# Performance work log

Measured on AMD Instinct MI355X. Metric: run time of the kernel, lower is better.

## Reference

```python
import jax, jax.numpy as jnp
import numpy as np

DN = ('NCDHW', 'OIDHW', 'NCDHW')

def conv3d(x, w, b):
    # kernel (1,3,3), stride 1, padding (0,1,1)
    y = jax.lax.conv_general_dilated(x, w, window_strides=(1, 1, 1),
                                     padding=[(0, 0), (1, 1), (1, 1)],
                                     dimension_numbers=DN)
    return y + b[None, :, None, None, None]

def setup_inputs() -> dict:
    key = jax.random.key(0)
    ks = jax.random.split(key, 9)
    B, C, S, H, W = 16, 64, 64, 32, 32
    Cd = C // 2
    fan = C * 9
    sc = 1.0 / np.sqrt(fan)
    x = jax.random.normal(ks[0], (B, C, S, H, W), jnp.float32)
    wq = jax.random.normal(ks[1], (Cd, C, 1, 3, 3), jnp.float32) * sc
    bq = jax.random.normal(ks[2], (Cd,), jnp.float32) * sc
    wk = jax.random.normal(ks[3], (Cd, C, 1, 3, 3), jnp.float32) * sc
    bk = jax.random.normal(ks[4], (Cd,), jnp.float32) * sc
    wv = jax.random.normal(ks[5], (Cd, C, 1, 3, 3), jnp.float32) * sc
    bv = jax.random.normal(ks[6], (Cd,), jnp.float32) * sc
    wo = jax.random.normal(ks[7], (C, Cd, 1, 3, 3), jnp.float32) * (1.0 / np.sqrt(Cd * 9))
    bo = jax.random.normal(ks[8], (C,), jnp.float32) * (1.0 / np.sqrt(Cd * 9))
    return {"x": x, "wq": wq, "bq": bq, "wk": wk, "bk": bk,
            "wv": wv, "bv": bv, "wo": wo, "bo": bo}

def reference(x, wq, bq, wk, bk, wv, bv, wo, bo):
    B, C, S, H, W = x.shape
    scale = (H * W) ** (-0.5)
    q = conv3d(x, wq, bq).reshape(B, -1, S, H * W)  # (B, Cd, S, HW)
    k = conv3d(x, wk, bk).reshape(B, -1, S, H * W)
    v = conv3d(x, wv, bv).reshape(B, -1, S, H * W)
    # per-channel attention over sequence dim with sigmoid gate
    attn = jax.nn.sigmoid(jnp.einsum('bcsf,bctf->bcst', q, k) * scale)  # (B, Cd, S, S)
    out = jnp.einsum('bcst,bctf->bcsf', attn, v)  # (B, Cd, S, HW)
    out = out.reshape(B, -1, S, H, W)
    return conv3d(out, wo, bo)
```

## Files before the change

kernel.cpp:

```cpp
#include <hip/hip_runtime.h>
#include <hip/hip_bf16.h>

#define BB   16
#define CC   64
#define SS   64
#define HWHW 1024
#define CD   32
#define QELEMS (BB * CD * SS * HWHW)

typedef unsigned short ushort_t;
typedef __attribute__((ext_vector_type(8)))  short bf16x8;
typedef __attribute__((ext_vector_type(16))) float f32x16;

static __device__ inline float bf2f(ushort_t u) {
    union { float f; unsigned int i; } v;
    v.i = ((unsigned int)u) << 16;
    return v.f;
}
static __device__ inline ushort_t f2bf(float f) {
    union { float f; unsigned int i; } v;
    v.f = f;
    unsigned int x = v.i;
    return (ushort_t)((x + 0x7fffu + ((x >> 16) & 1u)) >> 16);
}

__global__ __launch_bounds__(256) void pack_weights(
    const float* __restrict__ wq, const float* __restrict__ wk,
    const float* __restrict__ wv, const float* __restrict__ wo,
    ushort_t* __restrict__ wt, ushort_t* __restrict__ wt2)
{
    const int d = blockIdx.x * 256 + threadIdx.x;
    if (d < 9 * 96 * 64) {
        const int tap = d / (96 * 64);
        const int rem = d % (96 * 64);
        const int oc  = rem >> 6;
        const int c   = rem & 63;
        const float* wsrc = (oc < 32) ? wq : (oc < 64) ? wk : wv;
        const int ocl = oc & 31;
        wt[d] = f2bf(wsrc[((size_t)ocl * 64 + c) * 9 + tap]);
    }
    const int d2 = d - 9 * 96 * 64;
    if (d2 >= 0 && d2 < 9 * 64 * 32) {
        const int tap = d2 / (64 * 32);
        const int rem = d2 % (64 * 32);
        const int oc  = rem >> 5;
        const int c   = rem & 31;
        wt2[d2] = f2bf(wo[((size_t)oc * 32 + c) * 9 + tap]);
    }
}

__global__ __launch_bounds__(256) void transpose_x(
    const float* __restrict__ x, ushort_t* __restrict__ xT)
{
    __shared__ ushort_t t[64][132];

    const int bs  = blockIdx.x;
    const int b   = bs >> 6;
    const int s   = bs & 63;
    const int tid = threadIdx.x;
    const float* xb = x + ((size_t)b * CC * SS + s) * HWHW;
    ushort_t*    xo = xT + (size_t)bs * HWHW * CC;

    for (int fc = 0; fc < 8; ++fc) {
        __syncthreads();
#pragma unroll
        for (int i = 0; i < 8; ++i) {
            const int u  = tid + i * 256;
            const int c  = u >> 5;
            const int f4 = u & 31;
            const float4 v = *(const float4*)(xb + (size_t)c * SS * HWHW + fc * 128 + f4 * 4);
            const unsigned int lo = (unsigned int)f2bf(v.x) | ((unsigned int)f2bf(v.y) << 16);
            const unsigned int hi = (unsigned int)f2bf(v.z) | ((unsigned int)f2bf(v.w) << 16);
            *(uint2*)&t[c][f4 * 4] = make_uint2(lo, hi);
        }
        __syncthreads();
#pragma unroll
        for (int i = 0; i < 4; ++i) {
            const int u  = tid + i * 256;
            const int px = u >> 3;
            const int cg = (u & 7) * 8;
            bf16x8 vv;
#pragma unroll
            for (int j = 0; j < 8; ++j) vv[j] = (short)t[cg + j][px];
            *(bf16x8*)(xo + (size_t)(fc * 128 + px) * CC + cg) = vv;
        }
    }
}

__global__ __launch_bounds__(256) void transpose_att(
    const ushort_t* __restrict__ att, ushort_t* __restrict__ attT)
{
    __shared__ ushort_t t[32][260];

    const int bs  = blockIdx.x;
    const int b   = bs >> 6;
    const int s   = bs & 63;
    const int tid = threadIdx.x;
    const ushort_t* ab = att + ((size_t)b * CD * SS + s) * HWHW;
    ushort_t*       ao = attT + (size_t)bs * HWHW * CD;

    for (int fc = 0; fc < 4; ++fc) {
        __syncthreads();
#pragma unroll
        for (int i = 0; i < 8; ++i) {
            const int u  = tid + i * 256;
            const int c  = u >> 6;
            const int f4 = u & 63;
            const ushort4 v = *(const ushort4*)(ab + (size_t)c * SS * HWHW + fc * 256 + f4 * 4);
            *(ushort4*)&t[c][f4 * 4] = v;
        }
        __syncthreads();
#pragma unroll
        for (int i = 0; i < 4; ++i) {
            const int u  = tid + i * 256;
            const int px = u >> 2;
            const int cg = (u & 3) * 8;
            bf16x8 vv;
#pragma unroll
            for (int j = 0; j < 8; ++j) vv[j] = (short)t[cg + j][px];
            *(bf16x8*)(ao + (size_t)(fc * 256 + px) * CD + cg) = vv;
        }
    }
}

__global__ __launch_bounds__(256) void conv_qkv_mfma(
    const ushort_t* __restrict__ xT,
    const ushort_t* __restrict__ wt,
    const float* __restrict__ bq, const float* __restrict__ bk,
    const float* __restrict__ bv,
    ushort_t* __restrict__ qkv)
{
    __shared__ ushort_t xs[10][34][72];

    const int tid   = threadIdx.x;
    const int bs    = blockIdx.x >> 2;
    const int chunk = blockIdx.x & 3;
    const int b     = bs >> 6;
    const int s     = bs & 63;
    const int h0    = chunk * 8;

    if (tid < 160) {
        const int r    = tid >> 4;
        const int rest = tid & 15;
        const int col  = (rest >> 3) ? 33 : 0;
        const int c0   = (rest & 7) << 3;
        bf16x8 z = {0, 0, 0, 0, 0, 0, 0, 0};
        *(bf16x8*)&xs[r][col][c0] = z;
    }

    const ushort_t* xb = xT + (size_t)bs * HWHW * CC;
    {
        const int w  = tid >> 3;
        const int cg = (tid & 7) * 8;
#pragma unroll
        for (int it = 0; it < 10; ++it) {
            const int h = h0 - 1 + it;
            bf16x8 v = {0, 0, 0, 0, 0, 0, 0, 0};
            if (h >= 0 && h < 32)
                v = *(const bf16x8*)(xb + (size_t)(h * 32 + w) * CC + cg);
            *(bf16x8*)&xs[it][1 + w][cg] = v;
        }
    }
    __syncthreads();

    const int wvid = tid >> 6;
    const int lane = tid & 63;
    const int ln   = lane & 31;
    const int lh   = lane >> 5;
    const int nt0  = wvid * 2;

    f32x16 acc[3][2];
#pragma unroll
    for (int m = 0; m < 3; ++m)
#pragma unroll
        for (int n = 0; n < 2; ++n)
#pragma unroll
            for (int i = 0; i < 16; ++i) acc[m][n][i] = 0.f;

#pragma unroll 1
    for (int tap = 0; tap < 9; ++tap) {
        const int dh = tap / 3;
        const int dw = tap % 3;
        const ushort_t* wtap = wt + (size_t)tap * 96 * 64;
#pragma unroll
        for (int kc = 0; kc < 4; ++kc) {
            const int c0 = kc * 16 + lh * 8;
            const bf16x8 a0 = *(const bf16x8*)(wtap + (((size_t)ln      ) << 6) + c0);
            const bf16x8 a1 = *(const bf16x8*)(wtap + (((size_t)ln + 32 ) << 6) + c0);
            const bf16x8 a2 = *(const bf16x8*)(wtap + (((size_t)ln + 64 ) << 6) + c0);
            const bf16x8 b0 = *(const bf16x8*)&xs[nt0 + dh    ][ln + dw][c0];
            const bf16x8 b1 = *(const bf16x8*)&xs[nt0 + 1 + dh][ln + dw][c0];
            acc[0][0] = __builtin_amdgcn_mfma_f32_32x32x16_bf16(a0, b0, acc[0][0], 0, 0, 0);
            acc[0][1] = __builtin_amdgcn_mfma_f32_32x32x16_bf16(a0, b1, acc[0][1], 0, 0, 0);
            acc[1][0] = __builtin_amdgcn_mfma_f32_32x32x16_bf16(a1, b0, acc[1][0], 0, 0, 0);
            acc[1][1] = __builtin_amdgcn_mfma_f32_32x32x16_bf16(a1, b1, acc[1][1], 0, 0, 0);
            acc[2][0] = __builtin_amdgcn_mfma_f32_32x32x16_bf16(a2, b0, acc[2][0], 0, 0, 0);
            acc[2][1] = __builtin_amdgcn_mfma_f32_32x32x16_bf16(a2, b1, acc[2][1], 0, 0, 0);
        }
    }

    const float* biases[3] = {bq, bk, bv};
#pragma unroll
    for (int mt = 0; mt < 3; ++mt) {
        const float* bptr = biases[mt];
        ushort_t* dst = qkv + (size_t)mt * QELEMS + (((size_t)b * CD) * SS + s) * HWHW;
#pragma unroll
        for (int ntl = 0; ntl < 2; ++ntl) {
            const int gp = (h0 + nt0 + ntl) * 32 + ln;
#pragma unroll
            for (int r = 0; r < 16; ++r) {
                const int m = (r & 3) + 8 * (r >> 2) + 4 * lh;
                const float val = acc[mt][ntl][r] + bptr[m];
                dst[(size_t)m * SS * HWHW + gp] = f2bf(val);
            }
        }
    }
}

__global__ __launch_bounds__(256) void attn_kernel(ushort_t* __restrict__ qkv)
{
    __shared__ float    scb[64][65];
    __shared__ ushort_t qch[64][132];
    __shared__ ushort_t kch[64][132];

    const int tid = threadIdx.x;
    const int bc  = blockIdx.x;
    ushort_t* qbase = qkv + (size_t)bc * SS * HWHW;
    const ushort_t* kbase = qbase + QELEMS;
    const ushort_t* vbase = qbase + 2 * (size_t)QELEMS;

    const int ty = tid >> 4, tx = tid & 15;
    const int sy = ty * 4, sx = tx * 4;

    float acc[4][4];
#pragma unroll
    for (int i = 0; i < 4; ++i)
#pragma unroll
        for (int j = 0; j < 4; ++j) acc[i][j] = 0.0f;

    for (int fc = 0; fc < 8; ++fc) {
        __syncthreads();
#pragma unroll
        for (int u = 0; u < 8; ++u) {
            const int unit = tid + u * 256;
            const int row  = unit >> 5;
            const int col  = (unit & 31) * 4;
            const ushort4 qa = *(const ushort4*)(qbase + (size_t)row * HWHW + fc * 128 + col);
            const ushort4 ka = *(const ushort4*)(kbase + (size_t)row * HWHW + fc * 128 + col);
            *(ushort4*)&qch[row][col] = qa;
            *(ushort4*)&kch[row][col] = ka;
        }
        __syncthreads();

        for (int f = 0; f < 128; f += 2) {
            float q0[4], q1[4], k0[4], k1[4];
#pragma unroll
            for (int i = 0; i < 4; ++i) {
                const unsigned int qp = *(const unsigned int*)&qch[sy + i][f];
                q0[i] = bf2f((ushort_t)(qp & 0xffffu));
                q1[i] = bf2f((ushort_t)(qp >> 16));
                const unsigned int kp = *(const unsigned int*)&kch[sx + i][f];
                k0[i] = bf2f((ushort_t)(kp & 0xffffu));
                k1[i] = bf2f((ushort_t)(kp >> 16));
            }
#pragma unroll
            for (int i = 0; i < 4; ++i)
#pragma unroll
                for (int j = 0; j < 4; ++j)
                    acc[i][j] += q0[i] * k0[j] + q1[i] * k1[j];
        }
    }

    const float scale = 0.03125f;
#pragma unroll
    for (int i = 0; i < 4; ++i)
#pragma unroll
        for (int j = 0; j < 4; ++j) {
            const float xv = acc[i][j] * scale;
            scb[sy + i][sx + j] = 1.0f / (1.0f + __expf(-xv));
        }
    __syncthreads();

    const int fcol = tid * 4;
#pragma unroll 1
    for (int gIdx = 0; gIdx < 4; ++gIdx) {
        float o[16][4];
#pragma unroll
        for (int i = 0; i < 16; ++i)
#pragma unroll
            for (int j = 0; j < 4; ++j) o[i][j] = 0.0f;

        for (int t = 0; t < 64; ++t) {
            const ushort4 va = *(const ushort4*)(vbase + (size_t)t * HWHW + fcol);
            const float v0 = bf2f(va.x), v1 = bf2f(va.y), v2 = bf2f(va.z), v3 = bf2f(va.w);
#pragma unroll
            for (int i = 0; i < 16; ++i) {
                const float a = scb[gIdx * 16 + i][t];
                o[i][0] += a * v0;
                o[i][1] += a * v1;
                o[i][2] += a * v2;
                o[i][3] += a * v3;
            }
        }
#pragma unroll
        for (int i = 0; i < 16; ++i) {
            const int srow = gIdx * 16 + i;
            ushort4 u;
            u.x = f2bf(o[i][0]);
            u.y = f2bf(o[i][1]);
            u.z = f2bf(o[i][2]);
            u.w = f2bf(o[i][3]);
            *(ushort4*)(qbase + (size_t)srow * HWHW + fcol) = u;
        }
    }
}

__global__ __launch_bounds__(256) void conv_out_mfma(
    const ushort_t* __restrict__ attT,
    const ushort_t* __restrict__ wt2,
    const float* __restrict__ bo,
    float* __restrict__ out)
{
    __shared__ ushort_t xs[10][34][40];

    const int tid   = threadIdx.x;
    const int bs    = blockIdx.x >> 2;
    const int chunk = blockIdx.x & 3;
    const int b     = bs >> 6;
    const int s     = bs & 63;
    const int h0    = chunk * 8;

    if (tid < 80) {
        const int r    = tid >> 3;
        const int rest = tid & 7;
        const int col  = (rest >> 2) ? 33 : 0;
        const int c0   = (rest & 3) << 3;
        bf16x8 z = {0, 0, 0, 0, 0, 0, 0, 0};
        *(bf16x8*)&xs[r][col][c0] = z;
    }

    const ushort_t* ab = attT + (size_t)bs * HWHW * CD;
#pragma unroll
    for (int it = 0; it < 5; ++it) {
        const int u  = tid + it * 256;
        const int cg = (u & 3) * 8;
        const int w  = (u >> 2) & 31;
        const int r  = u >> 7;
        const int h  = h0 - 1 + r;
        bf16x8 v = {0, 0, 0, 0, 0, 0, 0, 0};
        if (h >= 0 && h < 32)
            v = *(const bf16x8*)(ab + (size_t)(h * 32 + w) * CD + cg);
        *(bf16x8*)&xs[r][1 + w][cg] = v;
    }
    __syncthreads();

    const int wvid = tid >> 6;
    const int lane = tid & 63;
    const int ln   = lane & 31;
    const int lh   = lane >> 5;
    const int nt0  = wvid * 2;

    f32x16 acc[2][2];
#pragma unroll
    for (int m = 0; m < 2; ++m)
#pragma unroll
        for (int n = 0; n < 2; ++n)
#pragma unroll
            for (int i = 0; i < 16; ++i) acc[m][n][i] = 0.f;

#pragma unroll 1
    for (int tap = 0; tap < 9; ++tap) {
        const int dh = tap / 3;
        const int dw = tap % 3;
        const ushort_t* wtap = wt2 + (size_t)tap * 64 * 32;
#pragma unroll
        for (int kc = 0; kc < 2; ++kc) {
            const int c0 = kc * 16 + lh * 8;
            const bf16x8 a0 = *(const bf16x8*)(wtap + (((size_t)ln      ) << 5) + c0);
            const bf16x8 a1 = *(const bf16x8*)(wtap + (((size_t)ln + 32 ) << 5) + c0);
            const bf16x8 b0 = *(const bf16x8*)&xs[nt0 + dh    ][ln + dw][c0];
            const bf16x8 b1 = *(const bf16x8*)&xs[nt0 + 1 + dh][ln + dw][c0];
            acc[0][0] = __builtin_amdgcn_mfma_f32_32x32x16_bf16(a0, b0, acc[0][0], 0, 0, 0);
            acc[0][1] = __builtin_amdgcn_mfma_f32_32x32x16_bf16(a0, b1, acc[0][1], 0, 0, 0);
            acc[1][0] = __builtin_amdgcn_mfma_f32_32x32x16_bf16(a1, b0, acc[1][0], 0, 0, 0);
            acc[1][1] = __builtin_amdgcn_mfma_f32_32x32x16_bf16(a1, b1, acc[1][1], 0, 0, 0);
        }
    }

#pragma unroll
    for (int mt = 0; mt < 2; ++mt) {
        float* dst = out + (((size_t)b * CC + mt * 32) * SS + s) * HWHW;
#pragma unroll
        for (int ntl = 0; ntl < 2; ++ntl) {
            const int gp = (h0 + nt0 + ntl) * 32 + ln;
#pragma unroll
            for (int r = 0; r < 16; ++r) {
                const int m = (r & 3) + 8 * (r >> 2) + 4 * lh;
                dst[(size_t)m * SS * HWHW + gp] = acc[mt][ntl][r] + bo[mt * 32 + m];
            }
        }
    }
}

extern "C" void kernel_launch(void* const* d_in, const int* in_sizes, int n_in,
                              void* d_out, int out_size, void* d_ws, size_t ws_size,
                              hipStream_t stream)
{
    const float* x  = (const float*)d_in[0];
    const float* wq = (const float*)d_in[1];
    const float* bq = (const float*)d_in[2];
    const float* wk = (const float*)d_in[3];
    const float* bk = (const float*)d_in[4];
    const float* wv = (const float*)d_in[5];
    const float* bv = (const float*)d_in[6];
    const float* wo = (const float*)d_in[7];
    const float* bo = (const float*)d_in[8];
    float* out = (float*)d_out;

    ushort_t* qkv = (ushort_t*)d_ws;
    ushort_t* wt  = (ushort_t*)((char*)d_ws + (size_t)3 * QELEMS * 2);
    ushort_t* wt2 = wt + 9 * 96 * 64;
    ushort_t* xT   = (ushort_t*)d_out;
    ushort_t* attT = qkv + (size_t)QELEMS;

    transpose_x<<<dim3(BB * SS), 256, 0, stream>>>(x, xT);
    pack_weights<<<288, 256, 0, stream>>>(wq, wk, wv, wo, wt, wt2);
    conv_qkv_mfma<<<dim3(BB * SS * 4), 256, 0, stream>>>(xT, wt, bq, bk, bv, qkv);
    attn_kernel<<<dim3(BB * CD), 256, 0, stream>>>(qkv);
    transpose_att<<<dim3(BB * SS), 256, 0, stream>>>(qkv, attT);
    conv_out_mfma<<<dim3(BB * SS * 4), 256, 0, stream>>>(attT, wt2, bo, out);
}
```

Before: 1.028 ms.

## Pre-swizzle weights and x, use direct global-to-LDS loads, vectorize attention

Weights are repacked into the per-lane MFMA fragment order, so each lane reads one contiguous 16-byte chunk. The transposed input is stored with an XOR channel swizzle, which lets the QKV conv load it straight into unpadded LDS with global_load_lds and read it back with fewer bank conflicts. Both conv kernels remap block IDs across 8 groups, presumably to spread work across XCDs, and set an occupancy hint of 3 blocks. The attention kernel switches to 16-byte bf16 LDS reads, a strided K-column assignment, and float4 reads of the score matrix. These are many separate changes, and the swizzle has to match exactly between the producer and consumer kernels.

After: 905.5 us. -11.9%, faster.

```diff
diff --git a/kernel.cpp b/kernel.cpp
--- a/kernel.cpp
+++ b/kernel.cpp
@@ -24,27 +24,38 @@
     return (ushort_t)((x + 0x7fffu + ((x >> 16) & 1u)) >> 16);
 }
 
+static __device__ inline void gload_lds16(const ushort_t* g, ushort_t* l) {
+    __builtin_amdgcn_global_load_lds(
+        (const __attribute__((address_space(1))) void*)g,
+        (__attribute__((address_space(3))) void*)l, 16, 0, 0);
+}
+
 __global__ __launch_bounds__(256) void pack_weights(
     const float* __restrict__ wq, const float* __restrict__ wk,
     const float* __restrict__ wv, const float* __restrict__ wo,
     ushort_t* __restrict__ wt, ushort_t* __restrict__ wt2)
 {
     const int d = blockIdx.x * 256 + threadIdx.x;
-    if (d < 9 * 96 * 64) {
-        const int tap = d / (96 * 64);
-        const int rem = d % (96 * 64);
-        const int oc  = rem >> 6;
-        const int c   = rem & 63;
-        const float* wsrc = (oc < 32) ? wq : (oc < 64) ? wk : wv;
-        const int ocl = oc & 31;
+    if (d < 9 * 3 * 4 * 512) {
+        const int e    = d & 7;
+        const int lane = (d >> 3) & 63;
+        const int kc   = (d >> 9) & 3;
+        const int mt   = (d >> 11) % 3;
+        const int tap  = d / 6144;
+        const int ocl  = lane & 31;
+        const int c    = kc * 16 + (lane >> 5) * 8 + e;
+        const float* wsrc = (mt == 0) ? wq : (mt == 1) ? wk : wv;
         wt[d] = f2bf(wsrc[((size_t)ocl * 64 + c) * 9 + tap]);
     }
-    const int d2 = d - 9 * 96 * 64;
-    if (d2 >= 0 && d2 < 9 * 64 * 32) {
-        const int tap = d2 / (64 * 32);
-        const int rem = d2 % (64 * 32);
-        const int oc  = rem >> 5;
-        const int c   = rem & 31;
+    const int d2 = d - 9 * 3 * 4 * 512;
+    if (d2 >= 0 && d2 < 9 * 2 * 2 * 512) {
+        const int e    = d2 & 7;
+        const int lane = (d2 >> 3) & 63;
+        const int kc   = (d2 >> 9) & 1;
+        const int mt   = (d2 >> 10) & 1;
+        const int tap  = d2 / 2048;
+        const int oc   = mt * 32 + (lane & 31);
+        const int c    = kc * 16 + (lane >> 5) * 8 + e;
         wt2[d2] = f2bf(wo[((size_t)oc * 32 + c) * 9 + tap]);
     }
 }
@@ -77,12 +88,13 @@
 #pragma unroll
         for (int i = 0; i < 4; ++i) {
             const int u  = tid + i * 256;
-            const int px = u >> 3;
-            const int cg = (u & 7) * 8;
+            const int px = fc * 128 + (u >> 3);
+            const int g  = u & 7;
             bf16x8 vv;
 #pragma unroll
-            for (int j = 0; j < 8; ++j) vv[j] = (short)t[cg + j][px];
-            *(bf16x8*)(xo + (size_t)(fc * 128 + px) * CC + cg) = vv;
+            for (int j = 0; j < 8; ++j) vv[j] = (short)t[g * 8 + j][u >> 3];
+            const int slot = g ^ ((1 + (px & 31)) & 7);
+            *(bf16x8*)(xo + (size_t)px * CC + slot * 8) = vv;
         }
     }
 }
@@ -123,51 +135,56 @@
     }
 }
 
-__global__ __launch_bounds__(256) void conv_qkv_mfma(
+__global__ __launch_bounds__(256, 3) void conv_qkv_mfma(
     const ushort_t* __restrict__ xT,
     const ushort_t* __restrict__ wt,
     const float* __restrict__ bq, const float* __restrict__ bk,
     const float* __restrict__ bv,
     ushort_t* __restrict__ qkv)
 {
-    __shared__ ushort_t xs[10][34][72];
-
-    const int tid   = threadIdx.x;
-    const int bs    = blockIdx.x >> 2;
-    const int chunk = blockIdx.x & 3;
+    __shared__ ushort_t xs[10 * 34 * 64];
+
+    const int tid  = threadIdx.x;
+    const int nwg8 = gridDim.x >> 3;
+    const int bid  = (blockIdx.x & 7) * nwg8 + (blockIdx.x >> 3);
+    const int bs    = bid >> 2;
+    const int chunk = bid & 3;
     const int b     = bs >> 6;
     const int s     = bs & 63;
     const int h0    = chunk * 8;
+
+    const int wvid = tid >> 6;
+    const int lane = tid & 63;
+    const int ln   = lane & 31;
+    const int lh   = lane >> 5;
 
     if (tid < 160) {
         const int r    = tid >> 4;
         const int rest = tid & 15;
         const int col  = (rest >> 3) ? 33 : 0;
-        const int c0   = (rest & 7) << 3;
+        const int g    = rest & 7;
         bf16x8 z = {0, 0, 0, 0, 0, 0, 0, 0};
-        *(bf16x8*)&xs[r][col][c0] = z;
+        *(bf16x8*)&xs[(r * 34 + col) * 64 + g * 8] = z;
     }
 
     const ushort_t* xb = xT + (size_t)bs * HWHW * CC;
     {
-        const int w  = tid >> 3;
-        const int cg = (tid & 7) * 8;
+        bf16x8 z = {0, 0, 0, 0, 0, 0, 0, 0};
 #pragma unroll
         for (int it = 0; it < 10; ++it) {
             const int h = h0 - 1 + it;
-            bf16x8 v = {0, 0, 0, 0, 0, 0, 0, 0};
-            if (h >= 0 && h < 32)
-                v = *(const bf16x8*)(xb + (size_t)(h * 32 + w) * CC + cg);
-            *(bf16x8*)&xs[it][1 + w][cg] = v;
+            const int lbase = (it * 34 + 1) * 64;
+            if (h >= 0 && h < 32) {
+                gload_lds16(xb + (size_t)h * 2048 + wvid * 512 + lane * 8,
+                            &xs[lbase + wvid * 512]);
+            } else {
+                *(bf16x8*)&xs[lbase + tid * 8] = z;
+            }
         }
     }
     __syncthreads();
 
-    const int wvid = tid >> 6;
-    const int lane = tid & 63;
-    const int ln   = lane & 31;
-    const int lh   = lane >> 5;
-    const int nt0  = wvid * 2;
+    const int nt0 = wvid * 2;
 
     f32x16 acc[3][2];
 #pragma unroll
@@ -176,20 +193,27 @@
         for (int n = 0; n < 2; ++n)
 #pragma unroll
             for (int i = 0; i < 16; ++i) acc[m][n][i] = 0.f;
+
+    const ushort_t* wl = wt + lane * 8;
 
 #pragma unroll 1
     for (int tap = 0; tap < 9; ++tap) {
         const int dh = tap / 3;
         const int dw = tap % 3;
-        const ushort_t* wtap = wt + (size_t)tap * 96 * 64;
+        const int col = ln + dw;
+        const int czx = (col & 7) << 3;
+        const int r0b = ((nt0 + dh) * 34 + col) * 64;
+        const int r1b = ((nt0 + 1 + dh) * 34 + col) * 64;
+        const int wofs = tap * 6144;
 #pragma unroll
         for (int kc = 0; kc < 4; ++kc) {
             const int c0 = kc * 16 + lh * 8;
-            const bf16x8 a0 = *(const bf16x8*)(wtap + (((size_t)ln      ) << 6) + c0);
-            const bf16x8 a1 = *(const bf16x8*)(wtap + (((size_t)ln + 32 ) << 6) + c0);
-            const bf16x8 a2 = *(const bf16x8*)(wtap + (((size_t)ln + 64 ) << 6) + c0);
-            const bf16x8 b0 = *(const bf16x8*)&xs[nt0 + dh    ][ln + dw][c0];
-            const bf16x8 b1 = *(const bf16x8*)&xs[nt0 + 1 + dh][ln + dw][c0];
+            const int cz = c0 ^ czx;
+            const bf16x8 a0 = *(const bf16x8*)(wl + wofs + kc * 512);
+            const bf16x8 a1 = *(const bf16x8*)(wl + wofs + kc * 512 + 2048);
+            const bf16x8 a2 = *(const bf16x8*)(wl + wofs + kc * 512 + 4096);
+            const bf16x8 b0 = *(const bf16x8*)&xs[r0b + cz];
+            const bf16x8 b1 = *(const bf16x8*)&xs[r1b + cz];
             acc[0][0] = __builtin_amdgcn_mfma_f32_32x32x16_bf16(a0, b0, acc[0][0], 0, 0, 0);
             acc[0][1] = __builtin_amdgcn_mfma_f32_32x32x16_bf16(a0, b1, acc[0][1], 0, 0, 0);
             acc[1][0] = __builtin_amdgcn_mfma_f32_32x32x16_bf16(a1, b0, acc[1][0], 0, 0, 0);
@@ -219,9 +243,9 @@
 
 __global__ __launch_bounds__(256) void attn_kernel(ushort_t* __restrict__ qkv)
 {
-    __shared__ float    scb[64][65];
-    __shared__ ushort_t qch[64][132];
-    __shared__ ushort_t kch[64][132];
+    __shared__ float    scb[64][68];
+    __shared__ ushort_t qch[64][136];
+    __shared__ ushort_t kch[64][136];
 
     const int tid = threadIdx.x;
     const int bc  = blockIdx.x;
@@ -230,7 +254,7 @@
     const ushort_t* vbase = qbase + 2 * (size_t)QELEMS;
 
     const int ty = tid >> 4, tx = tid & 15;
-    const int sy = ty * 4, sx = tx * 4;
+    const int sy = ty * 4;
 
     float acc[4][4];
 #pragma unroll
@@ -252,22 +276,27 @@
         }
         __syncthreads();
 
-        for (int f = 0; f < 128; f += 2) {
-            float q0[4], q1[4], k0[4], k1[4];
-#pragma unroll
-            for (int i = 0; i < 4; ++i) {
-                const unsigned int qp = *(const unsigned int*)&qch[sy + i][f];
-                q0[i] = bf2f((ushort_t)(qp & 0xffffu));
-                q1[i] = bf2f((ushort_t)(qp >> 16));
-                const unsigned int kp = *(const unsigned int*)&kch[sx + i][f];
-                k0[i] = bf2f((ushort_t)(kp & 0xffffu));
-                k1[i] = bf2f((ushort_t)(kp >> 16));
-            }
+        for (int f8 = 0; f8 < 16; ++f8) {
+            bf16x8 qv[4], kv[4];
+#pragma unroll
+            for (int i = 0; i < 4; ++i) qv[i] = *(const bf16x8*)&qch[sy + i][f8 * 8];
+#pragma unroll
+            for (int j = 0; j < 4; ++j) kv[j] = *(const bf16x8*)&kch[tx + 16 * j][f8 * 8];
+            float qf[4][8], kf[4][8];
 #pragma unroll
             for (int i = 0; i < 4; ++i)
 #pragma unroll
+                for (int e = 0; e < 8; ++e) {
+                    qf[i][e] = bf2f((ushort_t)qv[i][e]);
+                    kf[i][e] = bf2f((ushort_t)kv[i][e]);
+                }
+#pragma unroll
+            for (int i = 0; i < 4; ++i)
+#pragma unroll
                 for (int j = 0; j < 4; ++j)
-                    acc[i][j] += q0[i] * k0[j] + q1[i] * k1[j];
+#pragma unroll
+                    for (int e = 0; e < 8; ++e)
+                        acc[i][j] += qf[i][e] * kf[j][e];
         }
     }
 
@@ -277,7 +306,7 @@
 #pragma unroll
         for (int j = 0; j < 4; ++j) {
             const float xv = acc[i][j] * scale;
-            scb[sy + i][sx + j] = 1.0f / (1.0f + __expf(-xv));
+            scb[sy + i][tx + 16 * j] = 1.0f / (1.0f + __expf(-xv));
         }
     __syncthreads();
 
@@ -290,16 +319,20 @@
 #pragma unroll
             for (int j = 0; j < 4; ++j) o[i][j] = 0.0f;
 
-        for (int t = 0; t < 64; ++t) {
-            const ushort4 va = *(const ushort4*)(vbase + (size_t)t * HWHW + fcol);
-            const float v0 = bf2f(va.x), v1 = bf2f(va.y), v2 = bf2f(va.z), v3 = bf2f(va.w);
+        for (int t4 = 0; t4 < 16; ++t4) {
+            float vv[4][4];
+#pragma unroll
+            for (int tv = 0; tv < 4; ++tv) {
+                const ushort4 va = *(const ushort4*)(vbase + (size_t)(t4 * 4 + tv) * HWHW + fcol);
+                vv[tv][0] = bf2f(va.x); vv[tv][1] = bf2f(va.y);
+                vv[tv][2] = bf2f(va.z); vv[tv][3] = bf2f(va.w);
+            }
 #pragma unroll
             for (int i = 0; i < 16; ++i) {
-                const float a = scb[gIdx * 16 + i][t];
-                o[i][0] += a * v0;
-                o[i][1] += a * v1;
-                o[i][2] += a * v2;
-                o[i][3] += a * v3;
+                const float4 a = *(const float4*)&scb[gIdx * 16 + i][t4 * 4];
+#pragma unroll
+                for (int f = 0; f < 4; ++f)
+                    o[i][f] += a.x * vv[0][f] + a.y * vv[1][f] + a.z * vv[2][f] + a.w * vv[3][f];
             }
         }
 #pragma unroll
@@ -315,7 +348,7 @@
     }
 }
 
-__global__ __launch_bounds__(256) void conv_out_mfma(
+__global__ __launch_bounds__(256, 3) void conv_out_mfma(
     const ushort_t* __restrict__ attT,
     const ushort_t* __restrict__ wt2,
     const float* __restrict__ bo,
@@ -323,9 +356,11 @@
 {
     __shared__ ushort_t xs[10][34][40];
 
-    const int tid   = threadIdx.x;
-    const int bs    = blockIdx.x >> 2;
-    const int chunk = blockIdx.x & 3;
+    const int tid  = threadIdx.x;
+    const int nwg8 = gridDim.x >> 3;
+    const int bid  = (blockIdx.x & 7) * nwg8 + (blockIdx.x >> 3);
+    const int bs    = bid >> 2;
+    const int chunk = bid & 3;
     const int b     = bs >> 6;
     const int s     = bs & 63;
     const int h0    = chunk * 8;
@@ -368,16 +403,18 @@
 #pragma unroll
             for (int i = 0; i < 16; ++i) acc[m][n][i] = 0.f;
 
+    const ushort_t* wl2 = wt2 + lane * 8;
+
 #pragma unroll 1
     for (int tap = 0; tap < 9; ++tap) {
         const int dh = tap / 3;
         const int dw = tap % 3;
-        const ushort_t* wtap = wt2 + (size_t)tap * 64 * 32;
+        const int wofs = tap * 2048;
 #pragma unroll
         for (int kc = 0; kc < 2; ++kc) {
             const int c0 = kc * 16 + lh * 8;
-            const bf16x8 a0 = *(const bf16x8*)(wtap + (((size_t)ln      ) << 5) + c0);
-            const bf16x8 a1 = *(const bf16x8*)(wtap + (((size_t)ln + 32 ) << 5) + c0);
+            const bf16x8 a0 = *(const bf16x8*)(wl2 + wofs + kc * 512);
+            const bf16x8 a1 = *(const bf16x8*)(wl2 + wofs + kc * 512 + 1024);
             const bf16x8 b0 = *(const bf16x8*)&xs[nt0 + dh    ][ln + dw][c0];
             const bf16x8 b1 = *(const bf16x8*)&xs[nt0 + 1 + dh][ln + dw][c0];
             acc[0][0] = __builtin_amdgcn_mfma_f32_32x32x16_bf16(a0, b0, acc[0][0], 0, 0, 0);
```
